# Kernel tuning notes

Hardware: AMD Instinct MI355X
Metric: run time of the kernel (lower is better)

The kernel has to match this reference:

```python
import jax, jax.numpy as jnp
import numpy as np

V = 100000      # num nodes
E = 600000      # num edges (even: first half in-edges, second half out-edges)
D_IN = 128
D_OUT = 128
NREL2 = 100     # num_rel * 2
BN_EPS = 1e-5


def ccorr(a, b):
    # circular correlation along last dim: irfft(conj(rfft(a)) * rfft(b), n=d)
    d = a.shape[-1]
    return jnp.fft.irfft(jnp.conj(jnp.fft.rfft(a)) * jnp.fft.rfft(b), n=d).astype(a.dtype)


def setup_inputs() -> dict:
    key = jax.random.key(0)
    ks = jax.random.split(key, 12)
    return {
        "x": jax.random.normal(ks[0], (V, D_IN), dtype=jnp.float32),
        "rel_repr": jax.random.normal(ks[1], (NREL2, D_IN), dtype=jnp.float32),
        "edge_norm": jax.random.uniform(ks[2], (E,), dtype=jnp.float32),
        "in_w": jax.random.normal(ks[3], (D_IN, D_OUT), dtype=jnp.float32) * 0.05,
        "out_w": jax.random.normal(ks[4], (D_IN, D_OUT), dtype=jnp.float32) * 0.05,
        "loop_w": jax.random.normal(ks[5], (D_IN, D_OUT), dtype=jnp.float32) * 0.05,
        "w_rel": jax.random.normal(ks[6], (D_IN, D_OUT), dtype=jnp.float32) * 0.05,
        "loop_rel": jax.random.normal(ks[7], (1, D_IN), dtype=jnp.float32),
        "bias": jnp.zeros((D_OUT,), dtype=jnp.float32),
        "bn_gamma": jnp.ones((D_OUT,), dtype=jnp.float32),
        "bn_beta": jnp.zeros((D_OUT,), dtype=jnp.float32),
        "edge_src": jax.random.randint(ks[8], (E,), 0, V, dtype=jnp.int32),
        "edge_dst": jax.random.randint(ks[9], (E,), 0, V, dtype=jnp.int32),
        "edge_type": jax.random.randint(ks[10], (E,), 0, NREL2, dtype=jnp.int32),
    }


def reference(x, rel_repr, edge_norm, in_w, out_w, loop_w, w_rel, loop_rel,
              bias, bn_gamma, bn_beta, edge_src, edge_dst, edge_type):
    rel = rel_repr  # rel_wt is None (num_base=-1)
    # gather src features per edge and compose with relation embedding (corr)
    edge_data = ccorr(x[edge_src], rel[edge_type])             # [E, D_IN]
    half = edge_data.shape[0] // 2
    msg = jnp.concatenate(
        [edge_data[:half] @ in_w, edge_data[half:] @ out_w], axis=0
    ) * edge_norm[:, None]                                     # [E, D_OUT]
    # scatter-sum into destination nodes
    agg = jax.ops.segment_sum(msg, edge_dst, num_segments=V)   # [V, D_OUT]
    # self-loop term
    loop = ccorr(x, jnp.broadcast_to(loop_rel, x.shape)) @ loop_w
    h = (agg + loop) / 3.0 + bias
    # BatchNorm1d (training mode: batch stats, biased variance)
    mean = h.mean(axis=0)
    var = h.var(axis=0)
    h = (h - mean) * jax.lax.rsqrt(var + BN_EPS) * bn_gamma + bn_beta
    # act is identity; ltr=True -> project relations
    return h, rel @ w_rel
```

## Files before the change

kernel.cpp:

```cpp
#include <hip/hip_runtime.h>
#include <hip/hip_bf16.h>

#define D 128
constexpr int V_N    = 100000;
constexpr int E_N    = 600000;
constexpr int HALF_E = E_N / 2;
constexpr int NREL2  = 100;
constexpr int NBUCK  = 2 * NREL2;
constexpr float BN_EPS_F = 1e-5f;

constexpr int CHUNK  = 4096;
constexpr int NCHUNK = (E_N + CHUNK - 1) / CHUNK;

typedef short bf16x8  __attribute__((ext_vector_type(8)));
typedef float f32x16  __attribute__((ext_vector_type(16)));
typedef float f32x4v  __attribute__((ext_vector_type(4)));

constexpr size_t M_RSV    = 201ull * D * D * 4;
constexpr size_t M_OFF    = 0;
constexpr size_t HIST_OFF = 201ull * D * D * 2;
constexpr size_t COFF_OFF = HIST_OFF + (size_t)NBUCK * NCHUNK * 4;
constexpr size_t SS_OFF   = M_RSV;
constexpr size_t SD_OFF   = SS_OFF + (size_t)E_N * 4;
constexpr size_t SN_OFF   = SD_OFF + (size_t)E_N * 4;
constexpr size_t ZERO_OFF = SN_OFF + (size_t)E_N * 4;
constexpr size_t CNT_OFF  = ZERO_OFF;
constexpr size_t CS_OFF   = ZERO_OFF + 1024;
constexpr size_t CQ_OFF   = CS_OFF + 512;
constexpr size_t ZERO_BYTES = 2048;
constexpr size_t ST_OFF   = ZERO_OFF + ZERO_BYTES;

constexpr size_t MT_BYTES  = 201ull * D * D * 2;
constexpr size_t P_SS_OFF  = MT_BYTES;
constexpr size_t P_SD_OFF  = P_SS_OFF + (size_t)E_N * 4;
constexpr size_t P_SN_OFF  = P_SD_OFF + (size_t)E_N * 4;
constexpr size_t P_AGG_OFF = P_SN_OFF + (size_t)E_N * 4;
constexpr size_t AGG_BYTES = (size_t)V_N * D * 2;
constexpr size_t P_HIST_OFF = P_AGG_OFF;
constexpr size_t P_COFF_OFF = P_HIST_OFF + (size_t)NBUCK * NCHUNK * 4;
constexpr size_t P_CS_OFF  = P_AGG_OFF + AGG_BYTES;
constexpr size_t P_CQ_OFF  = P_CS_OFF + 512;
constexpr size_t P_CNT_OFF = P_CQ_OFF + 512;
constexpr size_t P_ST_OFF  = P_CNT_OFF + 1024;
constexpr size_t WS_NEED_PK = P_ST_OFF + 1024;

__device__ inline unsigned short f2bf(float f) {
    __hip_bfloat16 h = __float2bfloat16(f);
    return __builtin_bit_cast(unsigned short, h);
}
__device__ inline float bf2f(unsigned short u) {
    return __uint_as_float(((unsigned)u) << 16);
}

__device__ inline int bucket_of(int e, const int* __restrict__ etype) {
    return etype[e] + (e < HALF_E ? 0 : NREL2);
}

__global__ __launch_bounds__(256) void k_hist_chunk(const int* __restrict__ etype,
                                                    int* __restrict__ hist) {
    __shared__ int h[NBUCK];
    for (int i = threadIdx.x; i < NBUCK; i += 256) h[i] = 0;
    __syncthreads();
    int c = blockIdx.x;
    int e0 = c * CHUNK;
#pragma unroll
    for (int r = 0; r < CHUNK / 256; r++) {
        int e = e0 + r * 256 + threadIdx.x;
        if (e < E_N) atomicAdd(&h[bucket_of(e, etype)], 1);
    }
    __syncthreads();
    for (int b = threadIdx.x; b < NBUCK; b += 256) hist[b * NCHUNK + c] = h[b];
}

__global__ void k_scan_bucket(const int* __restrict__ hist, int* __restrict__ chunkoff,
                              int* __restrict__ counts) {
    int b = blockIdx.x, lane = threadIdx.x;
    int acc = 0;
    for (int base = 0; base < NCHUNK; base += 64) {
        int c = base + lane;
        int v = (c < NCHUNK) ? hist[b * NCHUNK + c] : 0;
        int s = v;
#pragma unroll
        for (int off = 1; off < 64; off <<= 1) {
            int t = __shfl(s, lane - off, 64);
            if (lane >= off) s += t;
        }
        if (c < NCHUNK) chunkoff[b * NCHUNK + c] = acc + (s - v);
        acc += __shfl(s, 63, 64);
    }
    if (lane == 0) counts[b] = acc;
}

__global__ void k_scan(const int* __restrict__ counts, int* __restrict__ starts) {
    __shared__ int s[256];
    int i = threadIdx.x;
    int v = (i < NBUCK) ? counts[i] : 0;
    s[i] = v;
    __syncthreads();
    for (int off = 1; off < 256; off <<= 1) {
        int t = (i >= off) ? s[i - off] : 0;
        __syncthreads();
        s[i] += t;
        __syncthreads();
    }
    if (i < NBUCK) starts[i] = s[i] - v;
    if (i == 255) starts[NBUCK] = s[255];
}

__global__ __launch_bounds__(256) void k_scatter2(
    const int* __restrict__ src, const int* __restrict__ dst,
    const float* __restrict__ norm, const int* __restrict__ etype,
    const int* __restrict__ starts, const int* __restrict__ chunkoff,
    int* __restrict__ ssrc, int* __restrict__ sdst, float* __restrict__ snorm) {
    __shared__ int h[NBUCK];
    __shared__ int sbase[NBUCK];
    int c = blockIdx.x;
    for (int b = threadIdx.x; b < NBUCK; b += 256) {
        h[b] = 0;
        sbase[b] = starts[b] + chunkoff[b * NCHUNK + c];
    }
    __syncthreads();
    int e0 = c * CHUNK;
#pragma unroll
    for (int r = 0; r < CHUNK / 256; r++) {
        int e = e0 + r * 256 + threadIdx.x;
        if (e < E_N) {
            int b = bucket_of(e, etype);
            int rank = atomicAdd(&h[b], 1);
            int p = sbase[b] + rank;
            ssrc[p] = src[e]; sdst[p] = dst[e]; snorm[p] = norm[e];
        }
    }
}

__global__ void k_build_M(const float* __restrict__ rel, const float* __restrict__ in_w,
                          const float* __restrict__ out_w, const float* __restrict__ loop_rel,
                          const float* __restrict__ loop_w, ushort* __restrict__ MT) {
    extern __shared__ float smem[];
    float* sW = smem;
    float* sR = smem + D * D;
    int b = blockIdx.x;
    const float* r = (b < NREL2) ? rel + (size_t)b * D
                   : (b < NBUCK) ? rel + (size_t)(b - NREL2) * D : loop_rel;
    const float* W = (b < NREL2) ? in_w : (b < NBUCK) ? out_w : loop_w;
    for (int i = threadIdx.x; i < D * D; i += blockDim.x) sW[i] = W[i];
    for (int i = threadIdx.x; i < D; i += blockDim.x) { float v = r[i]; sR[i] = v; sR[i + D] = v; }
    __syncthreads();
    int o  = threadIdx.x & 127;
    int jg = threadIdx.x >> 7;
    ushort* MTb = MT + (size_t)b * (D * D);
    for (int pass = 0; pass < 4; pass++) {
        int jbase = jg * 64 + pass * 16;
        float acc[16];
#pragma unroll
        for (int t = 0; t < 16; t++) acc[t] = 0.f;
        for (int k = 0; k < D; k++) {
            float w = sW[k * D + o];
#pragma unroll
            for (int t = 0; t < 16; t++) acc[t] += sR[jbase + t + k] * w;
        }
#pragma unroll
        for (int t = 0; t < 16; t++) MTb[(size_t)o * D + jbase + t] = f2bf(acc[t]);
    }
}

__global__ void k_relw(const float* __restrict__ rel, const float* __restrict__ w_rel,
                       float* __restrict__ out2) {
    int rr = blockIdx.x, o = threadIdx.x;
    float acc = 0.f;
    for (int k = 0; k < D; k++) acc += rel[rr * D + k] * w_rel[k * D + o];
    out2[rr * D + o] = acc;
}

constexpr int BPB = 8;

__global__ __launch_bounds__(256) void k_edge_pk(
    const float* __restrict__ x, const ushort* __restrict__ MT,
    const int* __restrict__ starts, const int* __restrict__ ssrc,
    const int* __restrict__ sdst, const float* __restrict__ snorm,
    ushort* __restrict__ agg) {
    int wid  = threadIdx.x >> 6, lane = threadIdx.x & 63;
    int l31  = lane & 31, l5 = lane >> 5;
    int bucket = blockIdx.x / BPB;
    int sib    = (blockIdx.x % BPB) * 2 + (wid >> 1);
    int oh     = wid & 1;
    int bstart = starts[bucket], bend = starts[bucket + 1];
    const ushort* MTb = MT + (size_t)bucket * (D * D);
    int c0 = oh * 64 + 2 * l31;
    bf16x8 B0[8], B1[8];
#pragma unroll
    for (int kc = 0; kc < 8; kc++) {
        B0[kc] = *(const bf16x8*)&MTb[(size_t)c0 * D + kc * 16 + l5 * 8];
        B1[kc] = *(const bf16x8*)&MTb[(size_t)(c0 + 1) * D + kc * 16 + l5 * 8];
    }
    for (int tbase = bstart + sib * 32; tbase < bend; tbase += BPB * 2 * 32) {
        int nv = bend - tbase; if (nv > 32) nv = 32;
        int sr = ssrc[tbase + (l31 < nv ? l31 : 0)];
        const float* xr = x + (size_t)sr * D + l5 * 8;
        bf16x8 A[8];
#pragma unroll
        for (int kc = 0; kc < 8; kc++) {
            f32x4v v0 = *(const f32x4v*)(xr + kc * 16);
            f32x4v v1 = *(const f32x4v*)(xr + kc * 16 + 4);
            union { bf16x8 v; ushort u[8]; } t;
            t.u[0] = f2bf(v0[0]); t.u[1] = f2bf(v0[1]); t.u[2] = f2bf(v0[2]); t.u[3] = f2bf(v0[3]);
            t.u[4] = f2bf(v1[0]); t.u[5] = f2bf(v1[1]); t.u[6] = f2bf(v1[2]); t.u[7] = f2bf(v1[3]);
            A[kc] = t.v;
        }
        f32x16 C0, C1;
#pragma unroll
        for (int i = 0; i < 16; i++) { C0[i] = 0.f; C1[i] = 0.f; }
#pragma unroll
        for (int kc = 0; kc < 8; kc++) {
            C0 = __builtin_amdgcn_mfma_f32_32x32x16_bf16(A[kc], B0[kc], C0, 0, 0, 0);
            C1 = __builtin_amdgcn_mfma_f32_32x32x16_bf16(A[kc], B1[kc], C1, 0, 0, 0);
        }
#pragma unroll
        for (int r = 0; r < 16; r++) {
            int rw = (r & 3) + 8 * (r >> 2) + 4 * l5;
            if (rw < nv) {
                float nm = snorm[tbase + rw];
                int   dv = sdst[tbase + rw];
                union { ushort u[2]; unsigned int w; } p;
                p.u[0] = f2bf(C0[r] * nm);
                p.u[1] = f2bf(C1[r] * nm);
                ushort* ap = agg + (size_t)dv * D + c0;
                asm volatile("global_atomic_pk_add_bf16 %0, %1, off"
                             :: "v"(ap), "v"(p.w) : "memory");
            }
        }
    }
}

__global__ __launch_bounds__(256) void k_edge(
    const float* __restrict__ x, const ushort* __restrict__ MT,
    const int* __restrict__ starts, const int* __restrict__ ssrc,
    const int* __restrict__ sdst, const float* __restrict__ snorm,
    float* __restrict__ out) {
    int wid  = threadIdx.x >> 6, lane = threadIdx.x & 63;
    int l31  = lane & 31, l5 = lane >> 5;
    int bucket = blockIdx.x / BPB;
    int sib    = (blockIdx.x % BPB) * 2 + (wid >> 1);
    int oh     = wid & 1;
    int bstart = starts[bucket], bend = starts[bucket + 1];
    const ushort* MTb = MT + (size_t)bucket * (D * D);
    int ocol0 = oh * 64 + l31, ocol1 = oh * 64 + 32 + l31;
    bf16x8 B0[8], B1[8];
#pragma unroll
    for (int kc = 0; kc < 8; kc++) {
        B0[kc] = *(const bf16x8*)&MTb[(size_t)ocol0 * D + kc * 16 + l5 * 8];
        B1[kc] = *(const bf16x8*)&MTb[(size_t)ocol1 * D + kc * 16 + l5 * 8];
    }
    for (int tbase = bstart + sib * 32; tbase < bend; tbase += BPB * 2 * 32) {
        int nv = bend - tbase; if (nv > 32) nv = 32;
        int sr = ssrc[tbase + (l31 < nv ? l31 : 0)];
        const float* xr = x + (size_t)sr * D + l5 * 8;
        bf16x8 A[8];
#pragma unroll
        for (int kc = 0; kc < 8; kc++) {
            f32x4v v0 = *(const f32x4v*)(xr + kc * 16);
            f32x4v v1 = *(const f32x4v*)(xr + kc * 16 + 4);
            union { bf16x8 v; ushort u[8]; } t;
            t.u[0] = f2bf(v0[0]); t.u[1] = f2bf(v0[1]); t.u[2] = f2bf(v0[2]); t.u[3] = f2bf(v0[3]);
            t.u[4] = f2bf(v1[0]); t.u[5] = f2bf(v1[1]); t.u[6] = f2bf(v1[2]); t.u[7] = f2bf(v1[3]);
            A[kc] = t.v;
        }
        f32x16 C0, C1;
#pragma unroll
        for (int i = 0; i < 16; i++) { C0[i] = 0.f; C1[i] = 0.f; }
#pragma unroll
        for (int kc = 0; kc < 8; kc++) {
            C0 = __builtin_amdgcn_mfma_f32_32x32x16_bf16(A[kc], B0[kc], C0, 0, 0, 0);
            C1 = __builtin_amdgcn_mfma_f32_32x32x16_bf16(A[kc], B1[kc], C1, 0, 0, 0);
        }
#pragma unroll
        for (int r = 0; r < 16; r++) {
            int rw = (r & 3) + 8 * (r >> 2) + 4 * l5;
            if (rw < nv) {
                float nm = snorm[tbase + rw];
                int   dv = sdst[tbase + rw];
                float* op = out + (size_t)dv * D;
                atomicAdd(op + ocol0, C0[r] * nm);
                atomicAdd(op + ocol1, C1[r] * nm);
            }
        }
    }
}

constexpr int LOOP_GRID = 400;
__global__ __launch_bounds__(256) void k_loop_pk(
    const float* __restrict__ x, const ushort* __restrict__ MT,
    const float* __restrict__ bias, const ushort* __restrict__ agg,
    float* __restrict__ out, float* __restrict__ colsum, float* __restrict__ colsq) {
    int wid = threadIdx.x >> 6, lane = threadIdx.x & 63;
    int l31 = lane & 31, l5 = lane >> 5;
    int oh  = wid & 1;
    int strm = blockIdx.x * 2 + (wid >> 1);
    const int NSTR = LOOP_GRID * 2;
    const ushort* MTb = MT + (size_t)NBUCK * (D * D);
    int ocol0 = oh * 64 + l31, ocol1 = oh * 64 + 32 + l31;
    bf16x8 B0[8], B1[8];
#pragma unroll
    for (int kc = 0; kc < 8; kc++) {
        B0[kc] = *(const bf16x8*)&MTb[(size_t)ocol0 * D + kc * 16 + l5 * 8];
        B1[kc] = *(const bf16x8*)&MTb[(size_t)ocol1 * D + kc * 16 + l5 * 8];
    }
    float b0 = bias[ocol0], b1 = bias[ocol1];
    float ps0 = 0.f, pq0 = 0.f, ps1 = 0.f, pq1 = 0.f;
    const int NT = V_N / 32;
    for (int tile = strm; tile < NT; tile += NSTR) {
        int tbase = tile * 32;
        const float* xr = x + (size_t)(tbase + l31) * D + l5 * 8;
        bf16x8 A[8];
#pragma unroll
        for (int kc = 0; kc < 8; kc++) {
            f32x4v v0 = *(const f32x4v*)(xr + kc * 16);
            f32x4v v1 = *(const f32x4v*)(xr + kc * 16 + 4);
            union { bf16x8 v; ushort u[8]; } t;
            t.u[0] = f2bf(v0[0]); t.u[1] = f2bf(v0[1]); t.u[2] = f2bf(v0[2]); t.u[3] = f2bf(v0[3]);
            t.u[4] = f2bf(v1[0]); t.u[5] = f2bf(v1[1]); t.u[6] = f2bf(v1[2]); t.u[7] = f2bf(v1[3]);
            A[kc] = t.v;
        }
        f32x16 C0, C1;
#pragma unroll
        for (int i = 0; i < 16; i++) { C0[i] = 0.f; C1[i] = 0.f; }
#pragma unroll
        for (int kc = 0; kc < 8; kc++) {
            C0 = __builtin_amdgcn_mfma_f32_32x32x16_bf16(A[kc], B0[kc], C0, 0, 0, 0);
            C1 = __builtin_amdgcn_mfma_f32_32x32x16_bf16(A[kc], B1[kc], C1, 0, 0, 0);
        }
#pragma unroll
        for (int r = 0; r < 16; r++) {
            int rw = (r & 3) + 8 * (r >> 2) + 4 * l5;
            size_t i0 = (size_t)(tbase + rw) * D + ocol0;
            size_t i1 = (size_t)(tbase + rw) * D + ocol1;
            float h0 = (bf2f(agg[i0]) + C0[r]) * (1.f / 3.f) + b0;
            float h1 = (bf2f(agg[i1]) + C1[r]) * (1.f / 3.f) + b1;
            out[i0] = h0; out[i1] = h1;
            ps0 += h0; pq0 += h0 * h0;
            ps1 += h1; pq1 += h1 * h1;
        }
    }
    atomicAdd(&colsum[ocol0], ps0); atomicAdd(&colsq[ocol0], pq0);
    atomicAdd(&colsum[ocol1], ps1); atomicAdd(&colsq[ocol1], pq1);
}

__global__ __launch_bounds__(256) void k_loop(
    const float* __restrict__ x, const ushort* __restrict__ MT,
    const float* __restrict__ bias, float* __restrict__ out,
    float* __restrict__ colsum, float* __restrict__ colsq) {
    int wid = threadIdx.x >> 6, lane = threadIdx.x & 63;
    int l31 = lane & 31, l5 = lane >> 5;
    int oh  = wid & 1;
    int strm = blockIdx.x * 2 + (wid >> 1);
    const int NSTR = LOOP_GRID * 2;
    const ushort* MTb = MT + (size_t)NBUCK * (D * D);
    int ocol0 = oh * 64 + l31, ocol1 = oh * 64 + 32 + l31;
    bf16x8 B0[8], B1[8];
#pragma unroll
    for (int kc = 0; kc < 8; kc++) {
        B0[kc] = *(const bf16x8*)&MTb[(size_t)ocol0 * D + kc * 16 + l5 * 8];
        B1[kc] = *(const bf16x8*)&MTb[(size_t)ocol1 * D + kc * 16 + l5 * 8];
    }
    float b0 = bias[ocol0], b1 = bias[ocol1];
    float ps0 = 0.f, pq0 = 0.f, ps1 = 0.f, pq1 = 0.f;
    const int NT = V_N / 32;
    for (int tile = strm; tile < NT; tile += NSTR) {
        int tbase = tile * 32;
        const float* xr = x + (size_t)(tbase + l31) * D + l5 * 8;
        bf16x8 A[8];
#pragma unroll
        for (int kc = 0; kc < 8; kc++) {
            f32x4v v0 = *(const f32x4v*)(xr + kc * 16);
            f32x4v v1 = *(const f32x4v*)(xr + kc * 16 + 4);
            union { bf16x8 v; ushort u[8]; } t;
            t.u[0] = f2bf(v0[0]); t.u[1] = f2bf(v0[1]); t.u[2] = f2bf(v0[2]); t.u[3] = f2bf(v0[3]);
            t.u[4] = f2bf(v1[0]); t.u[5] = f2bf(v1[1]); t.u[6] = f2bf(v1[2]); t.u[7] = f2bf(v1[3]);
            A[kc] = t.v;
        }
        f32x16 C0, C1;
#pragma unroll
        for (int i = 0; i < 16; i++) { C0[i] = 0.f; C1[i] = 0.f; }
#pragma unroll
        for (int kc = 0; kc < 8; kc++) {
            C0 = __builtin_amdgcn_mfma_f32_32x32x16_bf16(A[kc], B0[kc], C0, 0, 0, 0);
            C1 = __builtin_amdgcn_mfma_f32_32x32x16_bf16(A[kc], B1[kc], C1, 0, 0, 0);
        }
#pragma unroll
        for (int r = 0; r < 16; r++) {
            int rw = (r & 3) + 8 * (r >> 2) + 4 * l5;
            size_t i0 = (size_t)(tbase + rw) * D + ocol0;
            size_t i1 = (size_t)(tbase + rw) * D + ocol1;
            float h0 = (out[i0] + C0[r]) * (1.f / 3.f) + b0;
            float h1 = (out[i1] + C1[r]) * (1.f / 3.f) + b1;
            out[i0] = h0; out[i1] = h1;
            ps0 += h0; pq0 += h0 * h0;
            ps1 += h1; pq1 += h1 * h1;
        }
    }
    atomicAdd(&colsum[ocol0], ps0); atomicAdd(&colsq[ocol0], pq0);
    atomicAdd(&colsum[ocol1], ps1); atomicAdd(&colsq[ocol1], pq1);
}

__global__ void k_bn(float* __restrict__ out, const float* __restrict__ colsum,
                     const float* __restrict__ colsq, const float* __restrict__ gamma,
                     const float* __restrict__ beta) {
    const size_t N4 = (size_t)V_N * D / 4;
    size_t stride = (size_t)gridDim.x * blockDim.x;
    for (size_t q = (size_t)blockIdx.x * blockDim.x + threadIdx.x; q < N4; q += stride) {
        int c4 = (int)(q & 31);
        float4 s  = *(const float4*)&colsum[c4 * 4];
        float4 sq = *(const float4*)&colsq[c4 * 4];
        float4 g  = *(const float4*)&gamma[c4 * 4];
        float4 be = *(const float4*)&beta[c4 * 4];
        float4 h  = *(float4*)&out[q * 4];
        const float inv = 1.f / (float)V_N;
        float m0 = s.x * inv, m1 = s.y * inv, m2 = s.z * inv, m3 = s.w * inv;
        float r0 = rsqrtf(sq.x * inv - m0 * m0 + BN_EPS_F);
        float r1 = rsqrtf(sq.y * inv - m1 * m1 + BN_EPS_F);
        float r2 = rsqrtf(sq.z * inv - m2 * m2 + BN_EPS_F);
        float r3 = rsqrtf(sq.w * inv - m3 * m3 + BN_EPS_F);
        h.x = (h.x - m0) * r0 * g.x + be.x;
        h.y = (h.y - m1) * r1 * g.y + be.y;
        h.z = (h.z - m2) * r2 * g.z + be.z;
        h.w = (h.w - m3) * r3 * g.w + be.w;
        *(float4*)&out[q * 4] = h;
    }
}

extern "C" void kernel_launch(void* const* d_in, const int* in_sizes, int n_in,
                              void* d_out, int out_size, void* d_ws, size_t ws_size,
                              hipStream_t stream) {
    const float* x        = (const float*)d_in[0];
    const float* rel      = (const float*)d_in[1];
    const float* enorm    = (const float*)d_in[2];
    const float* in_w     = (const float*)d_in[3];
    const float* out_w    = (const float*)d_in[4];
    const float* loop_w   = (const float*)d_in[5];
    const float* w_rel    = (const float*)d_in[6];
    const float* loop_rel = (const float*)d_in[7];
    const float* bias     = (const float*)d_in[8];
    const float* gamma    = (const float*)d_in[9];
    const float* beta     = (const float*)d_in[10];
    const int*   esrc     = (const int*)d_in[11];
    const int*   edst     = (const int*)d_in[12];
    const int*   etype    = (const int*)d_in[13];
    float* out = (float*)d_out;
    char*  ws  = (char*)d_ws;

    int gM = 201, smem = (D * D + 256) * sizeof(float);

    if (ws_size >= WS_NEED_PK) {
        ushort* MT       = (ushort*)(ws + 0);
        int*    ssrc     = (int*)(ws + P_SS_OFF);
        int*    sdst     = (int*)(ws + P_SD_OFF);
        float*  snorm    = (float*)(ws + P_SN_OFF);
        ushort* aggbf    = (ushort*)(ws + P_AGG_OFF);
        int*    hist     = (int*)(ws + P_HIST_OFF);
        int*    chunkoff = (int*)(ws + P_COFF_OFF);
        float*  colsum   = (float*)(ws + P_CS_OFF);
        float*  colsq    = (float*)(ws + P_CQ_OFF);
        int*    counts   = (int*)(ws + P_CNT_OFF);
        int*    starts   = (int*)(ws + P_ST_OFF);

        hipMemsetAsync(ws + P_CS_OFF, 0, 1024, stream);

        k_hist_chunk<<<NCHUNK, 256, 0, stream>>>(etype, hist);
        k_scan_bucket<<<NBUCK, 64, 0, stream>>>(hist, chunkoff, counts);
        k_scan<<<1, 256, 0, stream>>>(counts, starts);
        k_scatter2<<<NCHUNK, 256, 0, stream>>>(esrc, edst, enorm, etype, starts, chunkoff,
                                               ssrc, sdst, snorm);
        hipMemsetAsync(ws + P_AGG_OFF, 0, AGG_BYTES, stream);

        k_build_M<<<gM, 256, smem, stream>>>(rel, in_w, out_w, loop_rel, loop_w, MT);
        k_relw<<<NREL2, D, 0, stream>>>(rel, w_rel, out + (size_t)V_N * D);

        k_edge_pk<<<NBUCK * BPB, 256, 0, stream>>>(x, MT, starts, ssrc, sdst, snorm, aggbf);
        k_loop_pk<<<LOOP_GRID, 256, 0, stream>>>(x, MT, bias, aggbf, out, colsum, colsq);
        k_bn<<<2048, 256, 0, stream>>>(out, colsum, colsq, gamma, beta);
    } else {
        ushort* MT       = (ushort*)(ws + M_OFF);
        int*    hist     = (int*)(ws + HIST_OFF);
        int*    chunkoff = (int*)(ws + COFF_OFF);
        int*    ssrc     = (int*)(ws + SS_OFF);
        int*    sdst     = (int*)(ws + SD_OFF);
        float*  snorm    = (float*)(ws + SN_OFF);
        int*    counts   = (int*)(ws + CNT_OFF);
        float*  colsum   = (float*)(ws + CS_OFF);
        float*  colsq    = (float*)(ws + CQ_OFF);
        int*    starts   = (int*)(ws + ST_OFF);

        hipMemsetAsync(out, 0, (size_t)V_N * D * sizeof(float), stream);
        hipMemsetAsync(ws + ZERO_OFF, 0, ZERO_BYTES, stream);

        k_hist_chunk<<<NCHUNK, 256, 0, stream>>>(etype, hist);
        k_scan_bucket<<<NBUCK, 64, 0, stream>>>(hist, chunkoff, counts);
        k_scan<<<1, 256, 0, stream>>>(counts, starts);
        k_scatter2<<<NCHUNK, 256, 0, stream>>>(esrc, edst, enorm, etype, starts, chunkoff,
                                               ssrc, sdst, snorm);

        k_build_M<<<gM, 256, smem, stream>>>(rel, in_w, out_w, loop_rel, loop_w, MT);
        k_relw<<<NREL2, D, 0, stream>>>(rel, w_rel, out + (size_t)V_N * D);

        k_edge<<<NBUCK * BPB, 256, 0, stream>>>(x, MT, starts, ssrc, sdst, snorm, out);
        k_loop<<<LOOP_GRID, 256, 0, stream>>>(x, MT, bias, out, colsum, colsq);
        k_bn<<<2048, 256, 0, stream>>>(out, colsum, colsq, gamma, beta);
    }
}
```

Measured before the change: 562.3 us.

## Replace atomic bf16 scatter with CSR segment-sum over staged edge messages

Builds a destination-sorted CSR (degree count, scan, permutation) and has the edge kernel write per-edge bf16 messages to a staging buffer. A per-node segment-sum kernel then reduces them without atomics, in chunks sized to the available workspace. It also pre-converts x to bf16 once so the edge and loop kernels load half the bytes, and enlarges the loop grid. The aim is to remove contended atomic traffic on the aggregation buffer, at the cost of extra kernels, a large message write/read and more workspace.

```diff
diff --git a/kernel.cpp b/kernel.cpp
--- a/kernel.cpp
+++ b/kernel.cpp
@@ -15,20 +15,7 @@
 typedef short bf16x8  __attribute__((ext_vector_type(8)));
 typedef float f32x16  __attribute__((ext_vector_type(16)));
 typedef float f32x4v  __attribute__((ext_vector_type(4)));
-
-constexpr size_t M_RSV    = 201ull * D * D * 4;
-constexpr size_t M_OFF    = 0;
-constexpr size_t HIST_OFF = 201ull * D * D * 2;
-constexpr size_t COFF_OFF = HIST_OFF + (size_t)NBUCK * NCHUNK * 4;
-constexpr size_t SS_OFF   = M_RSV;
-constexpr size_t SD_OFF   = SS_OFF + (size_t)E_N * 4;
-constexpr size_t SN_OFF   = SD_OFF + (size_t)E_N * 4;
-constexpr size_t ZERO_OFF = SN_OFF + (size_t)E_N * 4;
-constexpr size_t CNT_OFF  = ZERO_OFF;
-constexpr size_t CS_OFF   = ZERO_OFF + 1024;
-constexpr size_t CQ_OFF   = CS_OFF + 512;
-constexpr size_t ZERO_BYTES = 2048;
-constexpr size_t ST_OFF   = ZERO_OFF + ZERO_BYTES;
+typedef unsigned int uint32;
 
 constexpr size_t MT_BYTES  = 201ull * D * D * 2;
 constexpr size_t P_SS_OFF  = MT_BYTES;
@@ -44,12 +31,34 @@
 constexpr size_t P_ST_OFF  = P_CNT_OFF + 1024;
 constexpr size_t WS_NEED_PK = P_ST_OFF + 1024;
 
+constexpr size_t V3_MT    = 0;
+constexpr size_t V3_SS    = MT_BYTES;
+constexpr size_t V3_SD    = V3_SS + (size_t)E_N * 4;
+constexpr size_t V3_SN    = V3_SD + (size_t)E_N * 4;
+constexpr size_t V3_XBF   = V3_SN + (size_t)E_N * 4;
+constexpr size_t V3_AGG   = V3_XBF + (size_t)V_N * D * 2;
+constexpr size_t V3_DEG   = V3_AGG + AGG_BYTES;
+constexpr size_t V3_RP    = V3_DEG + (size_t)V_N * 4;
+constexpr size_t V3_CUR   = V3_RP + (size_t)(V_N + 16) * 4;
+constexpr size_t V3_EIDX  = V3_CUR + (size_t)V_N * 4;
+constexpr size_t V3_HIST  = V3_EIDX + (size_t)E_N * 4;
+constexpr size_t V3_COFF  = V3_HIST + (size_t)NBUCK * NCHUNK * 4;
+constexpr size_t V3_CNT   = V3_COFF + (size_t)NBUCK * NCHUNK * 4;
+constexpr size_t V3_START = V3_CNT + 1024;
+constexpr size_t V3_BSUM  = V3_START + 1024;
+constexpr size_t V3_CS    = V3_BSUM + 1024;
+constexpr size_t V3_CQ    = V3_CS + 512;
+constexpr size_t V3_MSG   = (V3_CQ + 512 + 255) & ~(size_t)255;
+
+constexpr int SCAN_ELEMS = 1024;
+constexpr int NSCANB = (V_N + SCAN_ELEMS - 1) / SCAN_ELEMS;
+
 __device__ inline unsigned short f2bf(float f) {
     __hip_bfloat16 h = __float2bfloat16(f);
     return __builtin_bit_cast(unsigned short, h);
 }
-__device__ inline float bf2f(unsigned short u) {
-    return __uint_as_float(((unsigned)u) << 16);
+__device__ inline float bf2f(unsigned int u) {
+    return __uint_as_float(u << 16);
 }
 
 __device__ inline int bucket_of(int e, const int* __restrict__ etype) {
@@ -131,6 +140,19 @@
             ssrc[p] = src[e]; sdst[p] = dst[e]; snorm[p] = norm[e];
         }
     }
+}
+
+__global__ __launch_bounds__(256) void k_xbf(const float* __restrict__ x,
+                                             ushort* __restrict__ xbf) {
+    const int N8 = V_N * D / 8;
+    int i = blockIdx.x * 256 + threadIdx.x;
+    if (i >= N8) return;
+    f32x4v v0 = *(const f32x4v*)&x[(size_t)i * 8];
+    f32x4v v1 = *(const f32x4v*)&x[(size_t)i * 8 + 4];
+    union { ushort u[8]; uint4 q; } t;
+    t.u[0] = f2bf(v0[0]); t.u[1] = f2bf(v0[1]); t.u[2] = f2bf(v0[2]); t.u[3] = f2bf(v0[3]);
+    t.u[4] = f2bf(v1[0]); t.u[5] = f2bf(v1[1]); t.u[6] = f2bf(v1[2]); t.u[7] = f2bf(v1[3]);
+    *(uint4*)&xbf[(size_t)i * 8] = t.q;
 }
 
 __global__ void k_build_M(const float* __restrict__ rel, const float* __restrict__ in_w,
@@ -172,7 +194,199 @@
     out2[rr * D + o] = acc;
 }
 
+__global__ __launch_bounds__(256) void k_deg(const int* __restrict__ sdst,
+                                             int* __restrict__ deg) {
+    int p = blockIdx.x * 256 + threadIdx.x;
+    if (p < E_N) atomicAdd(&deg[sdst[p]], 1);
+}
+
+__global__ __launch_bounds__(256) void k_scan1(const int* __restrict__ deg,
+                                               int* __restrict__ rowptr,
+                                               int* __restrict__ blocksum) {
+    __shared__ int s[256];
+    int blk = blockIdx.x, tid = threadIdx.x;
+    int base = blk * SCAN_ELEMS + tid * 4;
+    int v[4]; int tot = 0;
+#pragma unroll
+    for (int j = 0; j < 4; j++) { int i = base + j; v[j] = (i < V_N) ? deg[i] : 0; tot += v[j]; }
+    s[tid] = tot;
+    __syncthreads();
+    for (int off = 1; off < 256; off <<= 1) {
+        int t = (tid >= off) ? s[tid - off] : 0;
+        __syncthreads();
+        s[tid] += t;
+        __syncthreads();
+    }
+    int run = s[tid] - tot;
+#pragma unroll
+    for (int j = 0; j < 4; j++) { int i = base + j; if (i < V_N) rowptr[i] = run; run += v[j]; }
+    if (tid == 255) blocksum[blk] = s[255];
+}
+
+__global__ void k_scan2(int* __restrict__ blocksum) {
+    __shared__ int s[128];
+    int i = threadIdx.x;
+    int v = (i < NSCANB) ? blocksum[i] : 0;
+    s[i] = v;
+    __syncthreads();
+    for (int off = 1; off < 128; off <<= 1) {
+        int t = (i >= off) ? s[i - off] : 0;
+        __syncthreads();
+        s[i] += t;
+        __syncthreads();
+    }
+    if (i < NSCANB) blocksum[i] = s[i] - v;
+}
+
+__global__ __launch_bounds__(256) void k_scan3(int* __restrict__ rowptr,
+                                               const int* __restrict__ blocksum,
+                                               int* __restrict__ cursor) {
+    int i = blockIdx.x * 256 + threadIdx.x;
+    if (i < V_N) {
+        int r = rowptr[i] + blocksum[i >> 10];
+        rowptr[i] = r; cursor[i] = r;
+    }
+    if (i == 0) rowptr[V_N] = E_N;
+}
+
+__global__ __launch_bounds__(256) void k_perm(const int* __restrict__ sdst,
+                                              int* __restrict__ cursor,
+                                              int* __restrict__ eidx) {
+    int p = blockIdx.x * 256 + threadIdx.x;
+    if (p < E_N) {
+        int slot = atomicAdd(&cursor[sdst[p]], 1);
+        eidx[slot] = p;
+    }
+}
+
 constexpr int BPB = 8;
+
+__global__ __launch_bounds__(256) void k_edge_st(
+    const ushort* __restrict__ xbf, const ushort* __restrict__ MT,
+    const int* __restrict__ starts, const int* __restrict__ ssrc,
+    const float* __restrict__ snorm, uint32* __restrict__ msg32,
+    int lo, int hi) {
+    int wid  = threadIdx.x >> 6, lane = threadIdx.x & 63;
+    int l31  = lane & 31, l5 = lane >> 5;
+    int bucket = blockIdx.x / BPB;
+    int sib    = (blockIdx.x % BPB) * 2 + (wid >> 1);
+    int oh     = wid & 1;
+    int bstart = starts[bucket], bend = starts[bucket + 1];
+    if (bstart >= bend || bstart >= hi || bend <= lo) return;
+    const ushort* MTb = MT + (size_t)bucket * (D * D);
+    int c0 = oh * 64 + 2 * l31;
+    bf16x8 B0[8], B1[8];
+#pragma unroll
+    for (int kc = 0; kc < 8; kc++) {
+        B0[kc] = *(const bf16x8*)&MTb[(size_t)c0 * D + kc * 16 + l5 * 8];
+        B1[kc] = *(const bf16x8*)&MTb[(size_t)(c0 + 1) * D + kc * 16 + l5 * 8];
+    }
+    int t_first = (bstart > lo ? bstart : lo) & ~31;
+    if (t_first < lo) t_first = lo;
+    int t_end = bend < hi ? bend : hi;
+    for (int t = t_first + sib * 32; t < t_end; t += BPB * 2 * 32) {
+        int pa = t + l31;
+        bool va = (pa >= bstart) && (pa < bend);
+        int sr = ssrc[va ? pa : bstart];
+        const ushort* xr = xbf + (size_t)sr * D + l5 * 8;
+        bf16x8 A[8];
+#pragma unroll
+        for (int kc = 0; kc < 8; kc++) A[kc] = *(const bf16x8*)(xr + kc * 16);
+        f32x16 C0, C1;
+#pragma unroll
+        for (int i = 0; i < 16; i++) { C0[i] = 0.f; C1[i] = 0.f; }
+#pragma unroll
+        for (int kc = 0; kc < 8; kc++) {
+            C0 = __builtin_amdgcn_mfma_f32_32x32x16_bf16(A[kc], B0[kc], C0, 0, 0, 0);
+            C1 = __builtin_amdgcn_mfma_f32_32x32x16_bf16(A[kc], B1[kc], C1, 0, 0, 0);
+        }
+#pragma unroll
+        for (int r = 0; r < 16; r++) {
+            int rw = (r & 3) + 8 * (r >> 2) + 4 * l5;
+            int p = t + rw;
+            if (p >= bstart && p < bend) {
+                float nm = snorm[p];
+                uint32 u = (uint32)f2bf(C0[r] * nm) | ((uint32)f2bf(C1[r] * nm) << 16);
+                msg32[(size_t)(p - lo) * 64 + oh * 32 + l31] = u;
+            }
+        }
+    }
+}
+
+__global__ __launch_bounds__(256) void k_segsum(
+    const uint32* __restrict__ msg32, const int* __restrict__ eidx,
+    const int* __restrict__ rowptr, uint32* __restrict__ agg32,
+    int lo, int hi) {
+    int v = blockIdx.x * 4 + (threadIdx.x >> 6);
+    if (v >= V_N) return;
+    int lane = threadIdx.x & 63;
+    int s = rowptr[v], e = rowptr[v + 1];
+    float a0 = 0.f, a1 = 0.f; int cnt = 0;
+    for (int i = s; i < e; i++) {
+        int p = eidx[i];
+        if (p >= lo && p < hi) {
+            uint32 u = msg32[(size_t)(p - lo) * 64 + lane];
+            a0 += bf2f(u & 0xffffu); a1 += bf2f(u >> 16); cnt++;
+        }
+    }
+    if (cnt) {
+        size_t idx = (size_t)v * 64 + lane;
+        uint32 u = agg32[idx];
+        a0 += bf2f(u & 0xffffu); a1 += bf2f(u >> 16);
+        agg32[idx] = (uint32)f2bf(a0) | ((uint32)f2bf(a1) << 16);
+    }
+}
+
+constexpr int LOOP_GRID = 1563;
+__global__ __launch_bounds__(256) void k_loop_v3(
+    const ushort* __restrict__ xbf, const ushort* __restrict__ MT,
+    const float* __restrict__ bias, const ushort* __restrict__ agg,
+    float* __restrict__ out, float* __restrict__ colsum, float* __restrict__ colsq) {
+    int wid = threadIdx.x >> 6, lane = threadIdx.x & 63;
+    int l31 = lane & 31, l5 = lane >> 5;
+    int oh  = wid & 1;
+    int strm = blockIdx.x * 2 + (wid >> 1);
+    const int NSTR = LOOP_GRID * 2;
+    const ushort* MTb = MT + (size_t)NBUCK * (D * D);
+    int ocol0 = oh * 64 + l31, ocol1 = oh * 64 + 32 + l31;
+    bf16x8 B0[8], B1[8];
+#pragma unroll
+    for (int kc = 0; kc < 8; kc++) {
+        B0[kc] = *(const bf16x8*)&MTb[(size_t)ocol0 * D + kc * 16 + l5 * 8];
+        B1[kc] = *(const bf16x8*)&MTb[(size_t)ocol1 * D + kc * 16 + l5 * 8];
+    }
+    float b0 = bias[ocol0], b1 = bias[ocol1];
+    float ps0 = 0.f, pq0 = 0.f, ps1 = 0.f, pq1 = 0.f;
+    const int NT = V_N / 32;
+    for (int tile = strm; tile < NT; tile += NSTR) {
+        int tbase = tile * 32;
+        const ushort* xr = xbf + (size_t)(tbase + l31) * D + l5 * 8;
+        bf16x8 A[8];
+#pragma unroll
+        for (int kc = 0; kc < 8; kc++) A[kc] = *(const bf16x8*)(xr + kc * 16);
+        f32x16 C0, C1;
+#pragma unroll
+        for (int i = 0; i < 16; i++) { C0[i] = 0.f; C1[i] = 0.f; }
+#pragma unroll
+        for (int kc = 0; kc < 8; kc++) {
+            C0 = __builtin_amdgcn_mfma_f32_32x32x16_bf16(A[kc], B0[kc], C0, 0, 0, 0);
+            C1 = __builtin_amdgcn_mfma_f32_32x32x16_bf16(A[kc], B1[kc], C1, 0, 0, 0);
+        }
+#pragma unroll
+        for (int r = 0; r < 16; r++) {
+            int rw = (r & 3) + 8 * (r >> 2) + 4 * l5;
+            size_t i0 = (size_t)(tbase + rw) * D + ocol0;
+            size_t i1 = (size_t)(tbase + rw) * D + ocol1;
+            float h0 = (bf2f((uint32)agg[i0]) + C0[r]) * (1.f / 3.f) + b0;
+            float h1 = (bf2f((uint32)agg[i1]) + C1[r]) * (1.f / 3.f) + b1;
+            out[i0] = h0; out[i1] = h1;
+            ps0 += h0; pq0 += h0 * h0;
+            ps1 += h1; pq1 += h1 * h1;
+        }
+    }
+    atomicAdd(&colsum[ocol0], ps0); atomicAdd(&colsq[ocol0], pq0);
+    atomicAdd(&colsum[ocol1], ps1); atomicAdd(&colsq[ocol1], pq1);
+}
 
 __global__ __launch_bounds__(256) void k_edge_pk(
     const float* __restrict__ x, const ushort* __restrict__ MT,
@@ -232,62 +446,6 @@
     }
 }
 
-__global__ __launch_bounds__(256) void k_edge(
-    const float* __restrict__ x, const ushort* __restrict__ MT,
-    const int* __restrict__ starts, const int* __restrict__ ssrc,
-    const int* __restrict__ sdst, const float* __restrict__ snorm,
-    float* __restrict__ out) {
-    int wid  = threadIdx.x >> 6, lane = threadIdx.x & 63;
-    int l31  = lane & 31, l5 = lane >> 5;
-    int bucket = blockIdx.x / BPB;
-    int sib    = (blockIdx.x % BPB) * 2 + (wid >> 1);
-    int oh     = wid & 1;
-    int bstart = starts[bucket], bend = starts[bucket + 1];
-    const ushort* MTb = MT + (size_t)bucket * (D * D);
-    int ocol0 = oh * 64 + l31, ocol1 = oh * 64 + 32 + l31;
-    bf16x8 B0[8], B1[8];
-#pragma unroll
-    for (int kc = 0; kc < 8; kc++) {
-        B0[kc] = *(const bf16x8*)&MTb[(size_t)ocol0 * D + kc * 16 + l5 * 8];
-        B1[kc] = *(const bf16x8*)&MTb[(size_t)ocol1 * D + kc * 16 + l5 * 8];
-    }
-    for (int tbase = bstart + sib * 32; tbase < bend; tbase += BPB * 2 * 32) {
-        int nv = bend - tbase; if (nv > 32) nv = 32;
-        int sr = ssrc[tbase + (l31 < nv ? l31 : 0)];
-        const float* xr = x + (size_t)sr * D + l5 * 8;
-        bf16x8 A[8];
-#pragma unroll
-        for (int kc = 0; kc < 8; kc++) {
-            f32x4v v0 = *(const f32x4v*)(xr + kc * 16);
-            f32x4v v1 = *(const f32x4v*)(xr + kc * 16 + 4);
-            union { bf16x8 v; ushort u[8]; } t;
-            t.u[0] = f2bf(v0[0]); t.u[1] = f2bf(v0[1]); t.u[2] = f2bf(v0[2]); t.u[3] = f2bf(v0[3]);
-            t.u[4] = f2bf(v1[0]); t.u[5] = f2bf(v1[1]); t.u[6] = f2bf(v1[2]); t.u[7] = f2bf(v1[3]);
-            A[kc] = t.v;
-        }
-        f32x16 C0, C1;
-#pragma unroll
-        for (int i = 0; i < 16; i++) { C0[i] = 0.f; C1[i] = 0.f; }
-#pragma unroll
-        for (int kc = 0; kc < 8; kc++) {
-            C0 = __builtin_amdgcn_mfma_f32_32x32x16_bf16(A[kc], B0[kc], C0, 0, 0, 0);
-            C1 = __builtin_amdgcn_mfma_f32_32x32x16_bf16(A[kc], B1[kc], C1, 0, 0, 0);
-        }
-#pragma unroll
-        for (int r = 0; r < 16; r++) {
-            int rw = (r & 3) + 8 * (r >> 2) + 4 * l5;
-            if (rw < nv) {
-                float nm = snorm[tbase + rw];
-                int   dv = sdst[tbase + rw];
-                float* op = out + (size_t)dv * D;
-                atomicAdd(op + ocol0, C0[r] * nm);
-                atomicAdd(op + ocol1, C1[r] * nm);
-            }
-        }
-    }
-}
-
-constexpr int LOOP_GRID = 400;
 __global__ __launch_bounds__(256) void k_loop_pk(
     const float* __restrict__ x, const ushort* __restrict__ MT,
     const float* __restrict__ bias, const ushort* __restrict__ agg,
@@ -334,65 +492,8 @@
             int rw = (r & 3) + 8 * (r >> 2) + 4 * l5;
             size_t i0 = (size_t)(tbase + rw) * D + ocol0;
             size_t i1 = (size_t)(tbase + rw) * D + ocol1;
-            float h0 = (bf2f(agg[i0]) + C0[r]) * (1.f / 3.f) + b0;
-            float h1 = (bf2f(agg[i1]) + C1[r]) * (1.f / 3.f) + b1;
-            out[i0] = h0; out[i1] = h1;
-            ps0 += h0; pq0 += h0 * h0;
-            ps1 += h1; pq1 += h1 * h1;
-        }
-    }
-    atomicAdd(&colsum[ocol0], ps0); atomicAdd(&colsq[ocol0], pq0);
-    atomicAdd(&colsum[ocol1], ps1); atomicAdd(&colsq[ocol1], pq1);
-}
-
-__global__ __launch_bounds__(256) void k_loop(
-    const float* __restrict__ x, const ushort* __restrict__ MT,
-    const float* __restrict__ bias, float* __restrict__ out,
-    float* __restrict__ colsum, float* __restrict__ colsq) {
-    int wid = threadIdx.x >> 6, lane = threadIdx.x & 63;
-    int l31 = lane & 31, l5 = lane >> 5;
-    int oh  = wid & 1;
-    int strm = blockIdx.x * 2 + (wid >> 1);
-    const int NSTR = LOOP_GRID * 2;
-    const ushort* MTb = MT + (size_t)NBUCK * (D * D);
-    int ocol0 = oh * 64 + l31, ocol1 = oh * 64 + 32 + l31;
-    bf16x8 B0[8], B1[8];
-#pragma unroll
-    for (int kc = 0; kc < 8; kc++) {
-        B0[kc] = *(const bf16x8*)&MTb[(size_t)ocol0 * D + kc * 16 + l5 * 8];
-        B1[kc] = *(const bf16x8*)&MTb[(size_t)ocol1 * D + kc * 16 + l5 * 8];
-    }
-    float b0 = bias[ocol0], b1 = bias[ocol1];
-    float ps0 = 0.f, pq0 = 0.f, ps1 = 0.f, pq1 = 0.f;
-    const int NT = V_N / 32;
-    for (int tile = strm; tile < NT; tile += NSTR) {
-        int tbase = tile * 32;
-        const float* xr = x + (size_t)(tbase + l31) * D + l5 * 8;
-        bf16x8 A[8];
-#pragma unroll
-        for (int kc = 0; kc < 8; kc++) {
-            f32x4v v0 = *(const f32x4v*)(xr + kc * 16);
-            f32x4v v1 = *(const f32x4v*)(xr + kc * 16 + 4);
-            union { bf16x8 v; ushort u[8]; } t;
-            t.u[0] = f2bf(v0[0]); t.u[1] = f2bf(v0[1]); t.u[2] = f2bf(v0[2]); t.u[3] = f2bf(v0[3]);
-            t.u[4] = f2bf(v1[0]); t.u[5] = f2bf(v1[1]); t.u[6] = f2bf(v1[2]); t.u[7] = f2bf(v1[3]);
-            A[kc] = t.v;
-        }
-        f32x16 C0, C1;
-#pragma unroll
-        for (int i = 0; i < 16; i++) { C0[i] = 0.f; C1[i] = 0.f; }
-#pragma unroll
-        for (int kc = 0; kc < 8; kc++) {
-            C0 = __builtin_amdgcn_mfma_f32_32x32x16_bf16(A[kc], B0[kc], C0, 0, 0, 0);
-            C1 = __builtin_amdgcn_mfma_f32_32x32x16_bf16(A[kc], B1[kc], C1, 0, 0, 0);
-        }
-#pragma unroll
-        for (int r = 0; r < 16; r++) {
-            int rw = (r & 3) + 8 * (r >> 2) + 4 * l5;
-            size_t i0 = (size_t)(tbase + rw) * D + ocol0;
-            size_t i1 = (size_t)(tbase + rw) * D + ocol1;
-            float h0 = (out[i0] + C0[r]) * (1.f / 3.f) + b0;
-            float h1 = (out[i1] + C1[r]) * (1.f / 3.f) + b1;
+            float h0 = (bf2f((uint32)agg[i0]) + C0[r]) * (1.f / 3.f) + b0;
+            float h1 = (bf2f((uint32)agg[i1]) + C1[r]) * (1.f / 3.f) + b1;
             out[i0] = h0; out[i1] = h1;
             ps0 += h0; pq0 += h0 * h0;
             ps1 += h1; pq1 += h1 * h1;
@@ -448,62 +549,87 @@
     float* out = (float*)d_out;
     char*  ws  = (char*)d_ws;
 
-    int gM = 201, smem = (D * D + 256) * sizeof(float);
-
-    if (ws_size >= WS_NEED_PK) {
-        ushort* MT       = (ushort*)(ws + 0);
-        int*    ssrc     = (int*)(ws + P_SS_OFF);
-        int*    sdst     = (int*)(ws + P_SD_OFF);
-        float*  snorm    = (float*)(ws + P_SN_OFF);
-        ushort* aggbf    = (ushort*)(ws + P_AGG_OFF);
-        int*    hist     = (int*)(ws + P_HIST_OFF);
-        int*    chunkoff = (int*)(ws + P_COFF_OFF);
-        float*  colsum   = (float*)(ws + P_CS_OFF);
-        float*  colsq    = (float*)(ws + P_CQ_OFF);
-        int*    counts   = (int*)(ws + P_CNT_OFF);
-        int*    starts   = (int*)(ws + P_ST_OFF);
+    const int gM = 201, smem = (D * D + 256) * sizeof(float);
+    const int gE = (E_N + 255) / 256;
+
+    size_t msg_cap = ws_size > V3_MSG ? ws_size - V3_MSG : 0;
+    long cap_rows = (long)(msg_cap / 256) & ~31L;
+    bool use_v3 = cap_rows >= 75008;
+
+    if (use_v3) {
+        ushort* MT     = (ushort*)(ws + V3_MT);
+        int*    ssrc   = (int*)(ws + V3_SS);
+        int*    sdst   = (int*)(ws + V3_SD);
+        float*  snorm  = (float*)(ws + V3_SN);
+        ushort* xbf    = (ushort*)(ws + V3_XBF);
+        ushort* aggbf  = (ushort*)(ws + V3_AGG);
+        uint32* agg32  = (uint32*)(ws + V3_AGG);
+        int*    deg    = (int*)(ws + V3_DEG);
+        int*    rowptr = (int*)(ws + V3_RP);
+        int*    cursor = (int*)(ws + V3_CUR);
+        int*    eidx   = (int*)(ws + V3_EIDX);
+        int*    hist   = (int*)(ws + V3_HIST);
+        int*    coff   = (int*)(ws + V3_COFF);
+        int*    counts = (int*)(ws + V3_CNT);
+        int*    starts = (int*)(ws + V3_START);
+        int*    bsum   = (int*)(ws + V3_BSUM);
+        float*  colsum = (float*)(ws + V3_CS);
+        float*  colsq  = (float*)(ws + V3_CQ);
+        uint32* msg32  = (uint32*)(ws + V3_MSG);
+
+        hipMemsetAsync(ws + V3_AGG, 0, AGG_BYTES + (size_t)V_N * 4, stream);
+        hipMemsetAsync(ws + V3_CS, 0, 1024, stream);
+
+        k_hist_chunk<<<NCHUNK, 256, 0, stream>>>(etype, hist);
+        k_scan_bucket<<<NBUCK, 64, 0, stream>>>(hist, coff, counts);
+        k_scan<<<1, 256, 0, stream>>>(counts, starts);
+        k_scatter2<<<NCHUNK, 256, 0, stream>>>(esrc, edst, enorm, etype, starts, coff,
+                                               ssrc, sdst, snorm);
+        k_xbf<<<(V_N * D / 8 + 255) / 256, 256, 0, stream>>>(x, xbf);
+        k_build_M<<<gM, 256, smem, stream>>>(rel, in_w, out_w, loop_rel, loop_w, MT);
+        k_relw<<<NREL2, D, 0, stream>>>(rel, w_rel, out + (size_t)V_N * D);
+        k_deg<<<gE, 256, 0, stream>>>(sdst, deg);
+        k_scan1<<<NSCANB, 256, 0, stream>>>(deg, rowptr, bsum);
+        k_scan2<<<1, 128, 0, stream>>>(bsum);
+        k_scan3<<<(V_N + 255) / 256, 256, 0, stream>>>(rowptr, bsum, cursor);
+        k_perm<<<gE, 256, 0, stream>>>(sdst, cursor, eidx);
+
+        int S = (int)((E_N + cap_rows - 1) / cap_rows);
+        int range_len = (int)((((E_N + S - 1) / S) + 31) & ~31);
+        for (int sIdx = 0; sIdx < S; sIdx++) {
+            int lo = sIdx * range_len;
+            int hi = lo + range_len;
+            k_edge_st<<<NBUCK * BPB, 256, 0, stream>>>(xbf, MT, starts, ssrc, snorm,
+                                                       msg32, lo, hi);
+            k_segsum<<<(V_N + 3) / 4, 256, 0, stream>>>(msg32, eidx, rowptr, agg32, lo, hi);
+        }
+
+        k_loop_v3<<<LOOP_GRID, 256, 0, stream>>>(xbf, MT, bias, aggbf, out, colsum, colsq);
+        k_bn<<<2048, 256, 0, stream>>>(out, colsum, colsq, gamma, beta);
+    } else {
+        ushort* MT     = (ushort*)(ws + 0);
+        int*    ssrc   = (int*)(ws + P_SS_OFF);
+        int*    sdst   = (int*)(ws + P_SD_OFF);
+        float*  snorm  = (float*)(ws + P_SN_OFF);
+        ushort* aggbf  = (ushort*)(ws + P_AGG_OFF);
+        int*    hist   = (int*)(ws + P_HIST_OFF);
+        int*    coff   = (int*)(ws + P_COFF_OFF);
+        float*  colsum = (float*)(ws + P_CS_OFF);
+        float*  colsq  = (float*)(ws + P_CQ_OFF);
+        int*    counts = (int*)(ws + P_CNT_OFF);
+        int*    starts = (int*)(ws + P_ST_OFF);
 
         hipMemsetAsync(ws + P_CS_OFF, 0, 1024, stream);
-
         k_hist_chunk<<<NCHUNK, 256, 0, stream>>>(etype, hist);
-        k_scan_bucket<<<NBUCK, 64, 0, stream>>>(hist, chunkoff, counts);
+        k_scan_bucket<<<NBUCK, 64, 0, stream>>>(hist, coff, counts);
         k_scan<<<1, 256, 0, stream>>>(counts, starts);
-        k_scatter2<<<NCHUNK, 256, 0, stream>>>(esrc, edst, enorm, etype, starts, chunkoff,
+        k_scatter2<<<NCHUNK, 256, 0, stream>>>(esrc, edst, enorm, etype, starts, coff,
                                                ssrc, sdst, snorm);
         hipMemsetAsync(ws + P_AGG_OFF, 0, AGG_BYTES, stream);
-
         k_build_M<<<gM, 256, smem, stream>>>(rel, in_w, out_w, loop_rel, loop_w, MT);
         k_relw<<<NREL2, D, 0, stream>>>(rel, w_rel, out + (size_t)V_N * D);
-
         k_edge_pk<<<NBUCK * BPB, 256, 0, stream>>>(x, MT, starts, ssrc, sdst, snorm, aggbf);
         k_loop_pk<<<LOOP_GRID, 256, 0, stream>>>(x, MT, bias, aggbf, out, colsum, colsq);
         k_bn<<<2048, 256, 0, stream>>>(out, colsum, colsq, gamma, beta);
-    } else {
-        ushort* MT       = (ushort*)(ws + M_OFF);
-        int*    hist     = (int*)(ws + HIST_OFF);
-        int*    chunkoff = (int*)(ws + COFF_OFF);
-        int*    ssrc     = (int*)(ws + SS_OFF);
-        int*    sdst     = (int*)(ws + SD_OFF);
-        float*  snorm    = (float*)(ws + SN_OFF);
-        int*    counts   = (int*)(ws + CNT_OFF);
-        float*  colsum   = (float*)(ws + CS_OFF);
-        float*  colsq    = (float*)(ws + CQ_OFF);
-        int*    starts   = (int*)(ws + ST_OFF);
-
-        hipMemsetAsync(out, 0, (size_t)V_N * D * sizeof(float), stream);
-        hipMemsetAsync(ws + ZERO_OFF, 0, ZERO_BYTES, stream);
-
-        k_hist_chunk<<<NCHUNK, 256, 0, stream>>>(etype, hist);
-        k_scan_bucket<<<NBUCK, 64, 0, stream>>>(hist, chunkoff, counts);
-        k_scan<<<1, 256, 0, stream>>>(counts, starts);
-        k_scatter2<<<NCHUNK, 256, 0, stream>>>(esrc, edst, enorm, etype, starts, chunkoff,
-                                               ssrc, sdst, snorm);
-
-        k_build_M<<<gM, 256, smem, stream>>>(rel, in_w, out_w, loop_rel, loop_w, MT);
-        k_relw<<<NREL2, D, 0, stream>>>(rel, w_rel, out + (size_t)V_N * D);
-
-        k_edge<<<NBUCK * BPB, 256, 0, stream>>>(x, MT, starts, ssrc, sdst, snorm, out);
-        k_loop<<<LOOP_GRID, 256, 0, stream>>>(x, MT, bias, out, colsum, colsq);
-        k_bn<<<2048, 256, 0, stream>>>(out, colsum, colsq, gamma, beta);
-    }
-}
+    }
+}
```

New measurement: 898.1 us. 59.7% more time.
